# Kernel tuning notes

Hardware: AMD Instinct MI355X
Metric: run time of the kernel (lower is better)

## Reference

```python
import jax, jax.numpy as jnp
import numpy as np

# Config (matches init_kwargs)
B, T, N = 32, 512, 1024
FT, FS = 16, 32                 # max_time_F, max_space_F
NCH = FT * FS                   # n_channels = 512
MULT = 2
DIN = NCH * MULT                # input_dim = 1024
H = 1024                        # hidden_size
NCLS = 1                        # n_cls_tokens
NP = (T // FT) * (N // FS)      # n_patches = 1024
SCALE = float(H) ** 0.5         # config.scale is None -> hidden_size**0.5


def setup_inputs() -> dict:
    key = jax.random.key(0)
    k0, k1, k2, k3 = jax.random.split(key, 4)
    s = 0.02
    return {
        "spikes": jax.random.normal(k0, (B, T, N), dtype=jnp.float32),
        "W_embed": jax.random.normal(k1, (DIN, NCH), dtype=jnp.float32) * s,
        "b_embed": jnp.zeros((DIN,), dtype=jnp.float32),
        "cls_tokens": jnp.zeros((1, NCLS, DIN), dtype=jnp.float32),
        "W_proj": jax.random.normal(k2, (H, DIN), dtype=jnp.float32) * s,
        "b_proj": jnp.zeros((H,), dtype=jnp.float32),
        "pos_table": jax.random.normal(k3, (NP + NCLS, H), dtype=jnp.float32) * s,
    }


def reference(spikes, W_embed, b_embed, cls_tokens, W_proj, b_proj, pos_table):
    Bsz = spikes.shape[0]
    # Patchify: replaces the double python loop with one reshape/transpose.
    # [B,T,N] -> [B, T/FT, FT, N/FS, FS] -> [B, T/FT, N/FS, FT, FS] -> [B, NP, NCH]
    # flatten order (time-major within patch) matches torch's .flatten(1) on [B,FT,FS].
    patches = spikes.reshape(Bsz, T // FT, FT, N // FS, FS)
    patches = patches.transpose(0, 1, 3, 2, 4).reshape(Bsz, NP, NCH)
    # embed_spikes (linear)
    x = jnp.einsum("bpc,dc->bpd", patches, W_embed) + b_embed
    # prepend cls tokens
    cls = jnp.broadcast_to(cls_tokens, (Bsz, NCLS, DIN))
    x = jnp.concatenate([cls, x], axis=1)
    # act * scale, then projection
    x = jax.nn.gelu(x, approximate=False) * SCALE
    x = jnp.einsum("bpd,hd->bph", x, W_proj) + b_proj
    # positional embedding: stamps are arange, so direct table add
    stamp = jnp.broadcast_to(
        jnp.arange(NP + NCLS, dtype=jnp.int32)[None, :], (Bsz, NP + NCLS)
    )
    mask = jnp.ones((Bsz, NP + NCLS), dtype=jnp.int32)
    x = x + pos_table[None, :, :]
    # dropout p=0.0 -> identity
    return (x, mask, stamp)
```

## Files before the change

kernel.cpp:

```cpp
#include <hip/hip_runtime.h>
#include <stdint.h>


typedef __attribute__((ext_vector_type(8))) short bf16x8;
typedef __attribute__((ext_vector_type(4))) float f32x4;

#define VMCNT(n) asm volatile("s_waitcnt vmcnt(" #n ")" ::: "memory")
#define CFENCE() asm volatile("" ::: "memory")

__device__ __forceinline__ unsigned short f2bf(float f) {
  union { float f; unsigned u; } v; v.f = f;
  const unsigned u = v.u;
  return (unsigned short)((u + 0x7fffu + ((u >> 16) & 1u)) >> 16);
}

__device__ __forceinline__ float gelu_exact(float x) {
  return 0.5f * x * (1.0f + erff(x * 0.70710678118654752440f));
}

__device__ __forceinline__ void gl_lds16(const unsigned short* g, unsigned short* l) {
  __builtin_amdgcn_global_load_lds(
      (const __attribute__((address_space(1))) unsigned int*)g,
      (__attribute__((address_space(3))) unsigned int*)l, 16, 0, 0);
}


__global__ void cast_f32_bf16(const float* __restrict__ src,
                              unsigned short* __restrict__ dst, int n) {
  const int i = blockIdx.x * 256 + threadIdx.x;
  if (i < n) dst[i] = f2bf(src[i]);
}

__global__ void patchify(const float* __restrict__ spikes,
                         unsigned short* __restrict__ P) {
  const int idx = blockIdx.x * 256 + threadIdx.x;
  const int m = idx >> 7;
  const int c = (idx & 127) << 2;
  const int b = m >> 10, p = m & 1023;
  const int pt = p >> 5, ps = p & 31;
  const int ft = c >> 5, fs = c & 31;
  const float4 v = *(const float4*)(spikes +
      (size_t)(((b << 9) + pt * 16 + ft) << 10) + ps * 32 + fs);
  ushort4 o;
  o.x = f2bf(v.x); o.y = f2bf(v.y); o.z = f2bf(v.z); o.w = f2bf(v.w);
  *(ushort4*)(P + (size_t)m * 512 + c) = o;
}

__global__ void g0_and_pad(const float* __restrict__ cls,
                           unsigned short* __restrict__ G) {
  const int i = blockIdx.x * 256 + threadIdx.x;
  G[(size_t)32800 * 1024 + i] = 0;
  if (i < 1024) {
    const unsigned short bv = f2bf(gelu_exact(cls[i]) * 32.0f);
    for (int b = 0; b < 32; ++b) G[(size_t)(b * 1025) * 1024 + i] = bv;
  }
}

__global__ void mask_stamp(float* __restrict__ out) {
  const int i = blockIdx.x * 256 + threadIdx.x;
  if (i < 32800) {
    out[33587200 + i] = 1.0f;
    out[33587200 + 32800 + i] = (float)(i % 1025);
  }
}

__device__ __forceinline__ void stage_tile256(
    const unsigned short* __restrict__ A, const unsigned short* __restrict__ B,
    int K, int rowStart, int colStart, int rmax, int k0, int tid,
    unsigned short* la, unsigned short* lb) {
#pragma unroll
  for (int l = 0; l < 4; ++l) {
    const int g = l * 512 + tid;
    const int r = g >> 3;
    const int slot = g & 7;
    const int kc = (slot ^ (r & 7)) << 3;
    int ra = rowStart + r;
    if (ra > rmax) ra = rmax;
    gl_lds16(A + (size_t)ra * K + (k0 + kc), la + g * 8);
    gl_lds16(B + (size_t)(colStart + r) * K + (k0 + kc), lb + g * 8);
  }
}

template <int K, bool GELU_EPI>
__global__ __launch_bounds__(512, 2) void gemm_bt(
    const unsigned short* __restrict__ A, const unsigned short* __restrict__ B,
    const float* __restrict__ bias, unsigned short* __restrict__ Cg,
    float* __restrict__ Cf, const float* __restrict__ pos,
    int Mvalid, int rmax, int nRowBlk) {
  __shared__ __align__(16) unsigned short lsA[2][16384];
  __shared__ __align__(16) unsigned short lsB[2][16384];
  constexpr int NT = K / 64;

  const int tid = threadIdx.x;
  const int lane = tid & 63;
  const int w = tid >> 6;
  const int quad = lane >> 4;
  const int l16 = lane & 15;
  const int wm = (w >> 2) * 128;
  const int wn = (w & 3) * 64;

  const int nwg = nRowBlk * 4;
  const int q = nwg >> 3, rr = nwg & 7;
  const int xcd = blockIdx.x & 7, jj = blockIdx.x >> 3;
  const int wgid =
      (xcd < rr ? xcd * (q + 1) : rr * (q + 1) + (xcd - rr) * q) + jj;
  const int rowStart = (wgid >> 2) << 8;
  const int colStart = (wgid & 3) << 8;

  f32x4 acc[8][4];
  const f32x4 z = {0.f, 0.f, 0.f, 0.f};
#pragma unroll
  for (int i = 0; i < 8; ++i)
#pragma unroll
    for (int j = 0; j < 4; ++j) acc[i][j] = z;

  stage_tile256(A, B, K, rowStart, colStart, rmax, 0, tid, lsA[0], lsB[0]);

  const int aoff = (wm + l16) << 6;
  const int boff = (wn + l16) << 6;
  const int sl0 = (quad ^ (l16 & 7)) << 3;
  const int sl1 = ((4 + quad) ^ (l16 & 7)) << 3;

  for (int t = 0; t < NT; ++t) {
    const int cur = t & 1;
    if (t + 1 < NT) {
      stage_tile256(A, B, K, rowStart, colStart, rmax, (t + 1) * 64, tid,
                    lsA[cur ^ 1], lsB[cur ^ 1]);
      VMCNT(8);
    } else {
      VMCNT(0);
    }
    __builtin_amdgcn_s_barrier();
    CFENCE();

    const unsigned short* cA = lsA[cur];
    const unsigned short* cB = lsB[cur];

    {
      bf16x8 af[8], bf[4];
#pragma unroll
      for (int i = 0; i < 8; ++i)
        af[i] = *(const bf16x8*)(cA + aoff + i * 1024 + sl0);
#pragma unroll
      for (int j = 0; j < 4; ++j)
        bf[j] = *(const bf16x8*)(cB + boff + j * 1024 + sl0);
#pragma unroll
      for (int i = 0; i < 8; ++i)
#pragma unroll
        for (int j = 0; j < 4; ++j)
          acc[i][j] = __builtin_amdgcn_mfma_f32_16x16x32_bf16(af[i], bf[j],
                                                              acc[i][j], 0, 0, 0);
    }
    {
      bf16x8 af[8], bf[4];
#pragma unroll
      for (int i = 0; i < 8; ++i)
        af[i] = *(const bf16x8*)(cA + aoff + i * 1024 + sl1);
#pragma unroll
      for (int j = 0; j < 4; ++j)
        bf[j] = *(const bf16x8*)(cB + boff + j * 1024 + sl1);
#pragma unroll
      for (int i = 0; i < 8; ++i)
#pragma unroll
        for (int j = 0; j < 4; ++j)
          acc[i][j] = __builtin_amdgcn_mfma_f32_16x16x32_bf16(af[i], bf[j],
                                                              acc[i][j], 0, 0, 0);
    }

    CFENCE();
    __builtin_amdgcn_s_barrier();
    CFENCE();
  }

#pragma unroll
  for (int i = 0; i < 8; ++i) {
    const int rb = rowStart + wm + i * 16 + quad * 4;
#pragma unroll
    for (int j = 0; j < 4; ++j) {
      const int gc = colStart + wn + j * 16 + l16;
      const float bv = bias[gc];
#pragma unroll
      for (int r = 0; r < 4; ++r) {
        const int row = rb + r;
        float v = acc[i][j][r] + bv;
        if (GELU_EPI) {
          v = gelu_exact(v) * 32.0f;
          const int grow = row + (row >> 10) + 1;
          Cg[(size_t)grow * 1024 + gc] = f2bf(v);
        } else {
          if (row < Mvalid) {
            const int p = row % 1025;
            Cf[(size_t)row * 1024 + gc] = v + pos[(size_t)p * 1024 + gc];
          }
        }
      }
    }
  }
}


extern "C" void kernel_launch(void* const* d_in, const int* in_sizes, int n_in,
                              void* d_out, int out_size, void* d_ws, size_t ws_size,
                              hipStream_t stream) {
  const float* spikes  = (const float*)d_in[0];
  const float* W_embed = (const float*)d_in[1];
  const float* b_embed = (const float*)d_in[2];
  const float* cls     = (const float*)d_in[3];
  const float* W_proj  = (const float*)d_in[4];
  const float* b_proj  = (const float*)d_in[5];
  const float* pos     = (const float*)d_in[6];
  float* out = (float*)d_out;

  char* ws = (char*)d_ws;
  unsigned short* P  = (unsigned short*)(ws);
  unsigned short* G  = (unsigned short*)(ws + 33554432);
  unsigned short* WE = (unsigned short*)(ws + 100925440);
  unsigned short* WP = (unsigned short*)(ws + 101974016);

  hipLaunchKernelGGL(cast_f32_bf16, dim3(2048), dim3(256), 0, stream, W_embed, WE, 524288);
  hipLaunchKernelGGL(cast_f32_bf16, dim3(4096), dim3(256), 0, stream, W_proj, WP, 1048576);
  hipLaunchKernelGGL(patchify, dim3(16384), dim3(256), 0, stream, spikes, P);
  hipLaunchKernelGGL(g0_and_pad, dim3(384), dim3(256), 0, stream, cls, G);
  hipLaunchKernelGGL(mask_stamp, dim3(129), dim3(256), 0, stream, out);

  hipLaunchKernelGGL((gemm_bt<512, true>), dim3(512), dim3(512), 0, stream,
                     P, WE, b_embed, G, (float*)nullptr, (const float*)nullptr,
                     0, 32767, 128);
  hipLaunchKernelGGL((gemm_bt<1024, false>), dim3(516), dim3(512), 0, stream,
                     G, WP, b_proj, (unsigned short*)nullptr, out, pos,
                     32800, 32895, 129);
}
```

Baseline: 477.9 us.

## Split GEMM K-loop into half-tile stages with deeper LDS prefetch and setprio

Replaces the double-buffered 64-K tile staging with a four-slot ring of half tiles, loaded seven units ahead. Each K-step is split into four MFMA quadrants, with global-to-LDS loads issued between them so memory traffic overlaps compute. MFMA sections are wrapped in s_setprio. This adds several barriers per iteration and more complex vmcnt bookkeeping, and the LDS layout and the per-wave fragment indexing now depend on that ring.

```diff
diff --git a/kernel.cpp b/kernel.cpp
--- a/kernel.cpp
+++ b/kernel.cpp
@@ -6,7 +6,9 @@
 typedef __attribute__((ext_vector_type(4))) float f32x4;
 
 #define VMCNT(n) asm volatile("s_waitcnt vmcnt(" #n ")" ::: "memory")
+#define LGKM0()  asm volatile("s_waitcnt lgkmcnt(0)" ::: "memory")
 #define CFENCE() asm volatile("" ::: "memory")
+#define BARRIER() do { CFENCE(); __builtin_amdgcn_s_barrier(); CFENCE(); } while (0)
 
 __device__ __forceinline__ unsigned short f2bf(float f) {
   union { float f; unsigned u; } v; v.f = f;
@@ -64,20 +66,26 @@
   }
 }
 
-__device__ __forceinline__ void stage_tile256(
-    const unsigned short* __restrict__ A, const unsigned short* __restrict__ B,
-    int K, int rowStart, int colStart, int rmax, int k0, int tid,
-    unsigned short* la, unsigned short* lb) {
-#pragma unroll
-  for (int l = 0; l < 4; ++l) {
+__device__ __forceinline__ void stage_half(
+    int u, const unsigned short* __restrict__ A,
+    const unsigned short* __restrict__ B, int K, int rowStart, int colStart,
+    int rmax, int tid, unsigned short* lsA, unsigned short* lsB) {
+  const int t = u >> 2;
+  const int wch = u & 3;
+  const int hi = wch >> 1;
+  unsigned short* dst = ((wch & 1) ? lsB : lsA) + (((2 * t + hi) & 3) << 13);
+  const unsigned short* src = (wch & 1) ? B : A;
+  const int base = ((wch & 1) ? colStart : rowStart) + (hi << 7);
+  const int k0 = t << 6;
+#pragma unroll
+  for (int l = 0; l < 2; ++l) {
     const int g = l * 512 + tid;
     const int r = g >> 3;
-    const int slot = g & 7;
-    const int kc = (slot ^ (r & 7)) << 3;
-    int ra = rowStart + r;
-    if (ra > rmax) ra = rmax;
-    gl_lds16(A + (size_t)ra * K + (k0 + kc), la + g * 8);
-    gl_lds16(B + (size_t)(colStart + r) * K + (k0 + kc), lb + g * 8);
+    const int s8 = g & 7;
+    const int kc = (s8 ^ (r & 7)) << 3;
+    int row = base + r;
+    if (!(wch & 1) && row > rmax) row = rmax;
+    gl_lds16(src + (size_t)row * K + (k0 + kc), dst + g * 8);
   }
 }
 
@@ -87,9 +95,10 @@
     const float* __restrict__ bias, unsigned short* __restrict__ Cg,
     float* __restrict__ Cf, const float* __restrict__ pos,
     int Mvalid, int rmax, int nRowBlk) {
-  __shared__ __align__(16) unsigned short lsA[2][16384];
-  __shared__ __align__(16) unsigned short lsB[2][16384];
+  __shared__ __align__(16) unsigned short lsA[32768];
+  __shared__ __align__(16) unsigned short lsB[32768];
   constexpr int NT = K / 64;
+  constexpr int NH = 4 * NT;
 
   const int tid = threadIdx.x;
   const int lane = tid & 63;
@@ -114,62 +123,95 @@
 #pragma unroll
     for (int j = 0; j < 4; ++j) acc[i][j] = z;
 
-  stage_tile256(A, B, K, rowStart, colStart, rmax, 0, tid, lsA[0], lsB[0]);
-
-  const int aoff = (wm + l16) << 6;
-  const int boff = (wn + l16) << 6;
+  for (int u = 0; u < 7; ++u)
+    stage_half(u, A, B, K, rowStart, colStart, rmax, tid, lsA, lsB);
+  VMCNT(6);
+  BARRIER();
+
+  const int abase = l16 << 6;
+  const int bbase = ((wn & 64) + l16) << 6;
   const int sl0 = (quad ^ (l16 & 7)) << 3;
   const int sl1 = ((4 + quad) ^ (l16 & 7)) << 3;
 
   for (int t = 0; t < NT; ++t) {
-    const int cur = t & 1;
-    if (t + 1 < NT) {
-      stage_tile256(A, B, K, rowStart, colStart, rmax, (t + 1) * 64, tid,
-                    lsA[cur ^ 1], lsB[cur ^ 1]);
-      VMCNT(8);
-    } else {
-      VMCNT(0);
-    }
-    __builtin_amdgcn_s_barrier();
-    CFENCE();
-
-    const unsigned short* cA = lsA[cur];
-    const unsigned short* cB = lsB[cur];
-
-    {
-      bf16x8 af[8], bf[4];
-#pragma unroll
-      for (int i = 0; i < 8; ++i)
-        af[i] = *(const bf16x8*)(cA + aoff + i * 1024 + sl0);
-#pragma unroll
-      for (int j = 0; j < 4; ++j)
-        bf[j] = *(const bf16x8*)(cB + boff + j * 1024 + sl0);
-#pragma unroll
-      for (int i = 0; i < 8; ++i)
-#pragma unroll
-        for (int j = 0; j < 4; ++j)
-          acc[i][j] = __builtin_amdgcn_mfma_f32_16x16x32_bf16(af[i], bf[j],
-                                                              acc[i][j], 0, 0, 0);
-    }
-    {
-      bf16x8 af[8], bf[4];
-#pragma unroll
-      for (int i = 0; i < 8; ++i)
-        af[i] = *(const bf16x8*)(cA + aoff + i * 1024 + sl1);
-#pragma unroll
-      for (int j = 0; j < 4; ++j)
-        bf[j] = *(const bf16x8*)(cB + boff + j * 1024 + sl1);
-#pragma unroll
-      for (int i = 0; i < 8; ++i)
-#pragma unroll
-        for (int j = 0; j < 4; ++j)
-          acc[i][j] = __builtin_amdgcn_mfma_f32_16x16x32_bf16(af[i], bf[j],
-                                                              acc[i][j], 0, 0, 0);
-    }
-
-    CFENCE();
-    __builtin_amdgcn_s_barrier();
-    CFENCE();
+    const unsigned short* pa = lsA + (((2 * t + (w >> 2)) & 3) << 13) + abase;
+    const unsigned short* pb = lsB + (((2 * t + ((w >> 1) & 1)) & 3) << 13) + bbase;
+    bf16x8 a[8][2], b[4][2];
+
+#pragma unroll
+    for (int i = 0; i < 4; ++i) {
+      a[i][0] = *(const bf16x8*)(pa + i * 1024 + sl0);
+      a[i][1] = *(const bf16x8*)(pa + i * 1024 + sl1);
+    }
+#pragma unroll
+    for (int j = 0; j < 4; ++j) {
+      b[j][0] = *(const bf16x8*)(pb + j * 1024 + sl0);
+      b[j][1] = *(const bf16x8*)(pb + j * 1024 + sl1);
+    }
+    if (4 * t + 7 < NH)
+      stage_half(4 * t + 7, A, B, K, rowStart, colStart, rmax, tid, lsA, lsB);
+    BARRIER();
+    LGKM0();
+    __builtin_amdgcn_s_setprio(1);
+#pragma unroll
+    for (int i = 0; i < 4; ++i)
+#pragma unroll
+      for (int j = 0; j < 2; ++j) {
+        acc[i][j] = __builtin_amdgcn_mfma_f32_16x16x32_bf16(a[i][0], b[j][0], acc[i][j], 0, 0, 0);
+        acc[i][j] = __builtin_amdgcn_mfma_f32_16x16x32_bf16(a[i][1], b[j][1], acc[i][j], 0, 0, 0);
+      }
+    __builtin_amdgcn_s_setprio(0);
+    BARRIER();
+
+#pragma unroll
+    for (int i = 4; i < 8; ++i) {
+      a[i][0] = *(const bf16x8*)(pa + i * 1024 + sl0);
+      a[i][1] = *(const bf16x8*)(pa + i * 1024 + sl1);
+    }
+    BARRIER();
+    LGKM0();
+    __builtin_amdgcn_s_setprio(1);
+#pragma unroll
+    for (int i = 0; i < 4; ++i)
+#pragma unroll
+      for (int j = 2; j < 4; ++j) {
+        acc[i][j] = __builtin_amdgcn_mfma_f32_16x16x32_bf16(a[i][0], b[j][0], acc[i][j], 0, 0, 0);
+        acc[i][j] = __builtin_amdgcn_mfma_f32_16x16x32_bf16(a[i][1], b[j][1], acc[i][j], 0, 0, 0);
+      }
+    __builtin_amdgcn_s_setprio(0);
+    BARRIER();
+
+    if (4 * t + 8 < NH)
+      stage_half(4 * t + 8, A, B, K, rowStart, colStart, rmax, tid, lsA, lsB);
+    if (4 * t + 9 < NH)
+      stage_half(4 * t + 9, A, B, K, rowStart, colStart, rmax, tid, lsA, lsB);
+    BARRIER();
+    __builtin_amdgcn_s_setprio(1);
+#pragma unroll
+    for (int i = 4; i < 8; ++i)
+#pragma unroll
+      for (int j = 0; j < 2; ++j) {
+        acc[i][j] = __builtin_amdgcn_mfma_f32_16x16x32_bf16(a[i][0], b[j][0], acc[i][j], 0, 0, 0);
+        acc[i][j] = __builtin_amdgcn_mfma_f32_16x16x32_bf16(a[i][1], b[j][1], acc[i][j], 0, 0, 0);
+      }
+    __builtin_amdgcn_s_setprio(0);
+    BARRIER();
+
+    if (4 * t + 10 < NH)
+      stage_half(4 * t + 10, A, B, K, rowStart, colStart, rmax, tid, lsA, lsB);
+    if (t < NT - 2) { VMCNT(6); }
+    else if (t == NT - 2) { VMCNT(0); }
+    BARRIER();
+    __builtin_amdgcn_s_setprio(1);
+#pragma unroll
+    for (int i = 4; i < 8; ++i)
+#pragma unroll
+      for (int j = 2; j < 4; ++j) {
+        acc[i][j] = __builtin_amdgcn_mfma_f32_16x16x32_bf16(a[i][0], b[j][0], acc[i][j], 0, 0, 0);
+        acc[i][j] = __builtin_amdgcn_mfma_f32_16x16x32_bf16(a[i][1], b[j][1], acc[i][j], 0, 0, 0);
+      }
+    __builtin_amdgcn_s_setprio(0);
+    BARRIER();
   }
 
 #pragma unroll
```

New measurement: 479.6 us. Within noise of the previous version (+0.3%).
